# Optimization experiments

Measured on AMD Instinct MI355X. Metric: run time of the kernel, lower is better.

The kernel has to match this reference:

```python
import jax, jax.numpy as jnp
import numpy as np

NUM_HEADS = 1
HIDDEN = 256
HEAD_DIM = HIDDEN // NUM_HEADS
SCALE = HEAD_DIM ** -0.5


def _rotate_pairwise(x):
    # (... , d) -> rotate adjacent pairs: (x0,x1,x2,x3,..) -> (-x1,x0,-x3,x2,..)
    shape = x.shape
    x = x.reshape(*shape[:-1], -1, 2)
    x = jnp.stack([-x[..., 1], x[..., 0]], axis=-1)
    return x.reshape(shape)


def setup_inputs() -> dict:
    key = jax.random.key(0)
    ks = jax.random.split(key, 12)
    B, PB, QS, KS = 1, 1, 4096, 16448
    KV_IN = 64
    d = {
        'query': jax.random.normal(ks[0], (B, PB, QS, HIDDEN), jnp.float32),
        'key': jax.random.normal(ks[1], (B, PB, KS, KV_IN), jnp.float32),
        'value': jax.random.normal(ks[2], (B, PB, KS, KV_IN), jnp.float32),
        'rope_cos': jax.random.normal(ks[3], (QS, HEAD_DIM), jnp.float32),
        'rope_sin': jax.random.normal(ks[4], (QS, HEAD_DIM), jnp.float32),
        'wq': jax.random.normal(ks[5], (HIDDEN, HIDDEN), jnp.float32) * (HIDDEN ** -0.5),
        'bq': jnp.zeros((HIDDEN,), jnp.float32),
        'wk': jax.random.normal(ks[6], (KV_IN, HIDDEN), jnp.float32) * (KV_IN ** -0.5),
        'bk': jnp.zeros((HIDDEN,), jnp.float32),
        'wv': jax.random.normal(ks[7], (KV_IN, HIDDEN), jnp.float32) * (KV_IN ** -0.5),
        'bv': jnp.zeros((HIDDEN,), jnp.float32),
        'wo': jax.random.normal(ks[8], (HIDDEN, HIDDEN), jnp.float32) * (HIDDEN ** -0.5),
        'bo': jnp.zeros((HIDDEN,), jnp.float32),
        'num_k_exclude_rope': 64,
    }
    return d


def reference(query, key, value, rope_cos, rope_sin, wq, bq, wk, bk, wv, bv, wo, bo, num_k_exclude_rope):
    batch, pb, qs, _ = query.shape
    ks = key.shape[2]
    B = batch * pb
    # projections -> [B, H, S, hd]
    q = (query @ wq + bq).reshape(B, qs, NUM_HEADS, HEAD_DIM).transpose(0, 2, 1, 3)
    k = (key @ wk + bk).reshape(B, ks, NUM_HEADS, HEAD_DIM).transpose(0, 2, 1, 3)
    v = (value @ wv + bv).reshape(B, ks, NUM_HEADS, HEAD_DIM).transpose(0, 2, 1, 3)
    cos = rope_cos[None, None]  # [1,1,QS,hd]
    sin = rope_sin[None, None]
    # split off non-RoPE keys (object pointer tokens)
    n_rot = ks - num_k_exclude_rope
    k_rot, k_pass = k[:, :, :n_rot, :], k[:, :, n_rot:, :]
    q = q * cos + _rotate_pairwise(q) * sin
    if n_rot != qs:  # rope_k_repeat branch (static shapes)
        rep = n_rot // qs
        cos_k = jnp.repeat(cos, rep, axis=2)
        sin_k = jnp.repeat(sin, rep, axis=2)
    else:
        cos_k, sin_k = cos, sin
    k_emb = k_rot * cos_k + _rotate_pairwise(k_rot) * sin_k
    k = jnp.concatenate([k_emb, k_pass], axis=-2)
    attn = jax.nn.softmax(jnp.einsum('bhqd,bhkd->bhqk', q * SCALE, k), axis=-1)
    x = jnp.einsum('bhqk,bhkd->bhqd', attn, v)
    x = x.transpose(0, 2, 1, 3).reshape(batch, pb, qs, HIDDEN)
    return x @ wo + bo
```

## Files before the change

kernel.cpp:

```cpp
#include <hip/hip_runtime.h>
#include <hip/hip_bf16.h>

typedef __attribute__((ext_vector_type(4))) float floatx4;
typedef __attribute__((ext_vector_type(8))) short shortx8;
typedef __attribute__((ext_vector_type(8))) _Float16 halfx8;
typedef _Float16 half_t;

#define MFMA_BF16(A,B,C) __builtin_amdgcn_mfma_f32_16x16x32_bf16((A),(B),(C),0,0,0)
#define NEG_INF (-__builtin_inff())
#define GLOBAL_AS __attribute__((address_space(1)))
#define LDS_AS __attribute__((address_space(3)))

static __device__ __forceinline__ unsigned short f2b(float f) {
    union { float f; unsigned u; } v; v.f = f;
    unsigned r = v.u + 0x7FFFu + ((v.u >> 16) & 1u);
    return (unsigned short)(r >> 16);
}
static __device__ __forceinline__ unsigned pack_bf16(float lo, float hi) {
    return (unsigned)f2b(lo) | ((unsigned)f2b(hi) << 16);
}
static __device__ __forceinline__ unsigned pack_half(float lo, float hi) {
    union { half_t h[2]; unsigned u; } p;
    p.h[0] = (half_t)lo; p.h[1] = (half_t)hi;
    return p.u;
}
static __device__ __forceinline__ float EXP2F(float x) { return __builtin_amdgcn_exp2f(x); }

#define NSPLIT 8
#define NSPLIT_C 16
#define NTILES 257

__global__ __launch_bounds__(256) void wtrans_kernel(
    const float* __restrict__ wq, const float* __restrict__ wk,
    const float* __restrict__ wv, const float* __restrict__ wo,
    unsigned short* __restrict__ wqt, unsigned short* __restrict__ wkt,
    unsigned short* __restrict__ wvt, unsigned short* __restrict__ wot)
{
    __shared__ unsigned short tb[64 * 68];
    const int bid = blockIdx.x, tid = threadIdx.x;
    const float* src; unsigned short* dst; int K0, N0, Kfull;
    if (bid < 16)      { src = wq; dst = wqt; Kfull = 256; K0 = (bid >> 2) * 64; N0 = (bid & 3) * 64; }
    else if (bid < 20) { src = wk; dst = wkt; Kfull = 64;  K0 = 0; N0 = (bid - 16) * 64; }
    else if (bid < 24) { src = wv; dst = wvt; Kfull = 64;  K0 = 0; N0 = (bid - 20) * 64; }
    else { int t2 = bid - 24; src = wo; dst = wot; Kfull = 256; K0 = (t2 >> 2) * 64; N0 = (t2 & 3) * 64; }

    {
        const int r = tid >> 2, c0 = (tid & 3) * 16;
        const float* p = src + (K0 + r) * 256 + N0 + c0;
        #pragma unroll
        for (int j = 0; j < 16; j += 4) {
            floatx4 f = *(const floatx4*)(p + j);
            tb[r * 68 + c0 + j + 0] = f2b(f[0]);
            tb[r * 68 + c0 + j + 1] = f2b(f[1]);
            tb[r * 68 + c0 + j + 2] = f2b(f[2]);
            tb[r * 68 + c0 + j + 3] = f2b(f[3]);
        }
    }
    __syncthreads();
    {
        const int n = tid >> 2, k0 = (tid & 3) * 16;
        shortx8 v0, v1;
        #pragma unroll
        for (int j = 0; j < 8; j++) {
            v0[j] = tb[(k0 + j) * 68 + n];
            v1[j] = tb[(k0 + 8 + j) * 68 + n];
        }
        unsigned short* q = dst + (N0 + n) * Kfull + K0 + k0;
        *(shortx8*)q = v0;
        *(shortx8*)(q + 8) = v1;
    }
}

__global__ __launch_bounds__(256) void proj_kernel(
    const float* __restrict__ query, const float* __restrict__ key,
    const float* __restrict__ value,
    const unsigned short* __restrict__ wqt, const float* __restrict__ bq,
    const unsigned short* __restrict__ wkt, const float* __restrict__ bk,
    const unsigned short* __restrict__ wvt, const float* __restrict__ bv,
    const float* __restrict__ cosb, const float* __restrict__ sinb,
    const int* __restrict__ nkx,
    unsigned short* __restrict__ qr, unsigned short* __restrict__ krw,
    unsigned short* __restrict__ vtg)
{
    __shared__ unsigned short tbuf[256 * 72];
    const int tid = threadIdx.x;
    const int wave = tid >> 6, lane = tid & 63;
    const int c = lane & 15, quad = lane >> 4;
    const int bx = blockIdx.x;

    if (bx < 64) {
        const int m0 = bx * 64;
        shortx8 aA[8];
        {
            const int mrow = m0 + wave * 16 + c;
            #pragma unroll
            for (int ks = 0; ks < 8; ks++) {
                const float* p = query + mrow * 256 + ks * 32 + quad * 8;
                floatx4 f0 = *(const floatx4*)p;
                floatx4 f1 = *(const floatx4*)(p + 4);
                shortx8 a;
                #pragma unroll
                for (int j = 0; j < 4; j++) { a[j] = (short)f2b(f0[j]); a[j + 4] = (short)f2b(f1[j]); }
                aA[ks] = a;
            }
        }
        floatx4 acc[16];
        #pragma unroll
        for (int nt = 0; nt < 16; nt++) { acc[nt][0]=0.f; acc[nt][1]=0.f; acc[nt][2]=0.f; acc[nt][3]=0.f; }
        #pragma unroll
        for (int nt = 0; nt < 16; nt++) {
            #pragma unroll
            for (int ks = 0; ks < 8; ks++) {
                shortx8 b = *(const shortx8*)(wqt + (nt * 16 + c) * 256 + ks * 32 + quad * 8);
                acc[nt] = MFMA_BF16(aA[ks], b, acc[nt]);
            }
        }
        const float sc = 0.09016844005556021f;
        #pragma unroll
        for (int nt = 0; nt < 16; nt++) {
            const int col = nt * 16 + c;
            float vals[4];
            #pragma unroll
            for (int r = 0; r < 4; r++) {
                const int row = m0 + wave * 16 + quad * 4 + r;
                float v = acc[nt][r] + bq[col];
                float partner = __shfl_xor(v, 1);
                float cv = cosb[row * 256 + col];
                float sn = sinb[row * 256 + col];
                float rot = (col & 1) ? partner : -partner;
                vals[r] = (v * cv + rot * sn) * sc;
            }
            #pragma unroll
            for (int r2 = 0; r2 < 4; r2 += 2) {
                float a = vals[r2], b = vals[r2 + 1];
                float ax = __shfl_xor(a, 1), bx2 = __shfl_xor(b, 1);
                float lo = (c & 1) ? bx2 : a;
                float hi = (c & 1) ? b : ax;
                int row = m0 + wave * 16 + quad * 4 + r2 + (c & 1);
                *(unsigned*)(qr + row * 256 + nt * 16 + (c & ~1)) = pack_bf16(lo, hi);
            }
        }
        return;
    }

    const int isv = (bx >= 321);
    const int m0 = (isv ? (bx - 321) : (bx - 64)) * 64;
    const float* src = isv ? value : key;
    const unsigned short* wt = isv ? wvt : wkt;
    const float* bias = isv ? bv : bk;

    shortx8 aA[2];
    {
        const int mrow = m0 + wave * 16 + c;
        #pragma unroll
        for (int ks = 0; ks < 2; ks++) {
            const float* p = src + mrow * 64 + ks * 32 + quad * 8;
            floatx4 f0 = *(const floatx4*)p;
            floatx4 f1 = *(const floatx4*)(p + 4);
            shortx8 a;
            #pragma unroll
            for (int j = 0; j < 4; j++) { a[j] = (short)f2b(f0[j]); a[j + 4] = (short)f2b(f1[j]); }
            aA[ks] = a;
        }
    }
    floatx4 acc[16];
    #pragma unroll
    for (int nt = 0; nt < 16; nt++) { acc[nt][0]=0.f; acc[nt][1]=0.f; acc[nt][2]=0.f; acc[nt][3]=0.f; }
    #pragma unroll
    for (int nt = 0; nt < 16; nt++) {
        #pragma unroll
        for (int ks = 0; ks < 2; ks++) {
            shortx8 b = *(const shortx8*)(wt + (nt * 16 + c) * 64 + ks * 32 + quad * 8);
            acc[nt] = MFMA_BF16(aA[ks], b, acc[nt]);
        }
    }
    if (!isv) {
        const int n_rot = 16448 - nkx[0];
        int rep = n_rot / 4096; if (rep < 1) rep = 1;
        int rc4[4];
        #pragma unroll
        for (int r = 0; r < 4; r++) {
            int row = m0 + wave * 16 + quad * 4 + r;
            rc4[r] = row / rep;
        }
        #pragma unroll
        for (int nt = 0; nt < 16; nt++) {
            const int col = nt * 16 + c;
            float vals[4];
            #pragma unroll
            for (int r = 0; r < 4; r++) {
                const int row = m0 + wave * 16 + quad * 4 + r;
                float v = acc[nt][r] + bias[col];
                float partner = __shfl_xor(v, 1);
                float outv = v;
                if (row < n_rot) {
                    float cv = cosb[rc4[r] * 256 + col];
                    float sn = sinb[rc4[r] * 256 + col];
                    float rot = (col & 1) ? partner : -partner;
                    outv = v * cv + rot * sn;
                }
                vals[r] = outv;
            }
            #pragma unroll
            for (int r2 = 0; r2 < 4; r2 += 2) {
                float a = vals[r2], b = vals[r2 + 1];
                float ax = __shfl_xor(a, 1), bx2 = __shfl_xor(b, 1);
                float lo = (c & 1) ? bx2 : a;
                float hi = (c & 1) ? b : ax;
                int row = m0 + wave * 16 + quad * 4 + r2 + (c & 1);
                *(unsigned*)(krw + row * 256 + nt * 16 + (c & ~1)) = pack_bf16(lo, hi);
            }
        }
    } else {
        #pragma unroll
        for (int nt = 0; nt < 16; nt++) {
            const int col = nt * 16 + c;
            #pragma unroll
            for (int r = 0; r < 4; r++) {
                const int rl = wave * 16 + quad * 4 + r;
                tbuf[col * 72 + rl] = f2b(acc[nt][r] + bias[col]);
            }
        }
        __syncthreads();
        #pragma unroll
        for (int i = 0; i < 8; i++) {
            int G = i * 256 + tid;
            int n = G >> 3, g = G & 7;
            *(floatx4*)(vtg + n * 16448 + m0 + g * 8) = *(const floatx4*)(tbuf + n * 72 + g * 8);
        }
    }
}

__global__ __launch_bounds__(512, 2) void flash_kernel(
    const unsigned short* __restrict__ qr, const unsigned short* __restrict__ kr,
    const unsigned short* __restrict__ vt, half_t* __restrict__ Opart,
    float* __restrict__ Lpart)
{
    __shared__ unsigned short smem[75776];
    const int tid = threadIdx.x;
    const int wave = tid >> 6, lane = tid & 63;
    const int c = lane & 15, quad = lane >> 4;
    const int cx = c & 7;
    const int qg = wave & 3, kvh = wave >> 2;
    const int qrow0 = blockIdx.x * 128 + qg * 32;
    const int s = blockIdx.y;
    const int t0 = (s * NTILES) / NSPLIT, t1 = ((s + 1) * NTILES) / NSPLIT;
    unsigned short* pw = smem + 65536 + wave * 1280;

    shortx8 aQ[2][8];
    #pragma unroll
    for (int u = 0; u < 2; u++)
        #pragma unroll
        for (int ks = 0; ks < 8; ks++)
            aQ[u][ks] = *(const shortx8*)(qr + (qrow0 + u * 16 + c) * 256 + ks * 32 + quad * 8);

    floatx4 o[2][16];
    #pragma unroll
    for (int u = 0; u < 2; u++)
        #pragma unroll
        for (int nt = 0; nt < 16; nt++) { o[u][nt][0]=0.f; o[u][nt][1]=0.f; o[u][nt][2]=0.f; o[u][nt][3]=0.f; }
    float l_i[2] = { 0.f, 0.f };

    auto stage = [&](int t, int buf) {
        const int kv0 = t * 64;
        unsigned short* kb = smem + buf * 16384;
        unsigned short* vb = smem + 32768 + buf * 16384;
        #pragma unroll
        for (int i = 0; i < 4; i++) {
            int L = i * 512 + tid;
            int kv = L >> 5, p = L & 31;
            int g = (p & 24) | ((p & 7) ^ (kv & 7));
            __builtin_amdgcn_global_load_lds(
                (const GLOBAL_AS void*)(const void*)(kr + (kv0 + kv) * 256 + g * 8),
                (LDS_AS void*)(void*)(kb + (i * 512 + wave * 64) * 8), 16, 0, 0);
        }
        #pragma unroll
        for (int i = 0; i < 4; i++) {
            int L = i * 512 + tid;
            int d = L >> 3, p = L & 7;
            int g = p ^ (d & 7);
            __builtin_amdgcn_global_load_lds(
                (const GLOBAL_AS void*)(const void*)(vt + d * 16448 + kv0 + g * 8),
                (LDS_AS void*)(void*)(vb + (i * 512 + wave * 64) * 8), 16, 0, 0);
        }
    };

    stage(t0, 0);
    int cur = 0;
    const int pv_p = (kvh * 4 + quad) ^ cx;
    for (int t = t0; t < t1; t++) {
        __syncthreads();
        if (t + 1 < t1) stage(t + 1, cur ^ 1);
        const unsigned short* kb = smem + cur * 16384;
        const unsigned short* vb = smem + 32768 + cur * 16384;

        floatx4 sv[2][2];
        #pragma unroll
        for (int u = 0; u < 2; u++)
            #pragma unroll
            for (int nt = 0; nt < 2; nt++) { sv[u][nt][0]=0.f; sv[u][nt][1]=0.f; sv[u][nt][2]=0.f; sv[u][nt][3]=0.f; }
        #pragma unroll
        for (int nt = 0; nt < 2; nt++) {
            const unsigned short* krow = kb + (kvh * 32 + nt * 16 + c) * 256;
            #pragma unroll
            for (int ks = 0; ks < 8; ks++) {
                int p = ((ks >> 1) * 8) | ((((ks & 1) << 2) + quad) ^ cx);
                shortx8 kfrag = *(const shortx8*)(krow + p * 8);
                sv[0][nt] = MFMA_BF16(kfrag, aQ[0][ks], sv[0][nt]);
                sv[1][nt] = MFMA_BF16(kfrag, aQ[1][ks], sv[1][nt]);
            }
        }
        #pragma unroll
        for (int u = 0; u < 2; u++) {
            float rs = 0.f;
            #pragma unroll
            for (int nt = 0; nt < 2; nt++)
                #pragma unroll
                for (int r = 0; r < 4; r++) {
                    float pv = EXP2F(sv[u][nt][r]);
                    sv[u][nt][r] = pv;
                    rs += pv;
                }
            l_i[u] += rs;
        }
        #pragma unroll
        for (int u = 0; u < 2; u++)
            #pragma unroll
            for (int nt = 0; nt < 2; nt++)
                #pragma unroll
                for (int r2 = 0; r2 < 4; r2 += 2)
                    *(unsigned*)(pw + (u * 16 + c) * 40 + nt * 16 + quad * 4 + r2) =
                        pack_bf16(sv[u][nt][r2], sv[u][nt][r2 + 1]);
        shortx8 aP[2];
        #pragma unroll
        for (int u = 0; u < 2; u++)
            aP[u] = *(const shortx8*)(pw + (u * 16 + c) * 40 + quad * 8);
        #pragma unroll
        for (int nt = 0; nt < 16; nt++) {
            const unsigned short* vrow = vb + (nt * 16 + c) * 64;
            shortx8 b0 = *(const shortx8*)(vrow + pv_p * 8);
            o[0][nt] = MFMA_BF16(aP[0], b0, o[0][nt]);
            o[1][nt] = MFMA_BF16(aP[1], b0, o[1][nt]);
        }
        cur ^= 1;
    }
    const int sEff = s * 2 + kvh;
    half_t* Ob = Opart + (size_t)sEff * (4096 * 256);
    #pragma unroll
    for (int u = 0; u < 2; u++) {
        l_i[u] += __shfl_xor(l_i[u], 16);
        l_i[u] += __shfl_xor(l_i[u], 32);
    }
    float inv[2] = { 1.0f / l_i[0], 1.0f / l_i[1] };
    #pragma unroll
    for (int u = 0; u < 2; u++) {
        float ar[4];
        #pragma unroll
        for (int r = 0; r < 4; r++) ar[r] = __shfl(inv[u], quad * 4 + r);
        #pragma unroll
        for (int nt = 0; nt < 16; nt++) {
            o[u][nt][0] *= ar[0]; o[u][nt][1] *= ar[1];
            o[u][nt][2] *= ar[2]; o[u][nt][3] *= ar[3];
        }
    }
    #pragma unroll
    for (int u = 0; u < 2; u++)
        #pragma unroll
        for (int nt = 0; nt < 16; nt++)
            #pragma unroll
            for (int r2 = 0; r2 < 4; r2 += 2) {
                float a = o[u][nt][r2], b = o[u][nt][r2 + 1];
                float ax = __shfl_xor(a, 1), bx2 = __shfl_xor(b, 1);
                float lo = (c & 1) ? bx2 : a;
                float hi = (c & 1) ? b : ax;
                int row = qrow0 + u * 16 + quad * 4 + r2 + (c & 1);
                *(unsigned*)(Ob + row * 256 + nt * 16 + (c & ~1)) = pack_half(lo, hi);
            }
    if (quad == 0) {
        #pragma unroll
        for (int u = 0; u < 2; u++)
            Lpart[sEff * 4096 + qrow0 + u * 16 + c] = l_i[u];
    }
}

__global__ __launch_bounds__(256) void combine_kernel(
    const half_t* __restrict__ Opart, const float* __restrict__ Lpart,
    unsigned short* __restrict__ xb)
{
    int idx = blockIdx.x * 256 + threadIdx.x;
    int row = idx >> 5;
    int d0 = (idx & 31) * 8;
    float wn[NSPLIT_C], den = 0.f;
    #pragma unroll
    for (int sp = 0; sp < NSPLIT_C; sp++) { wn[sp] = Lpart[sp * 4096 + row]; den += wn[sp]; }
    float inv = 1.0f / den;
    #pragma unroll
    for (int sp = 0; sp < NSPLIT_C; sp++) wn[sp] *= inv;
    float acc[8];
    #pragma unroll
    for (int j = 0; j < 8; j++) acc[j] = 0.f;
    #pragma unroll
    for (int sp = 0; sp < NSPLIT_C; sp++) {
        halfx8 hv = *(const halfx8*)(Opart + (size_t)sp * (4096 * 256) + row * 256 + d0);
        #pragma unroll
        for (int j = 0; j < 8; j++) acc[j] += wn[sp] * (float)hv[j];
    }
    shortx8 xv;
    #pragma unroll
    for (int j = 0; j < 8; j++) xv[j] = (short)f2b(acc[j]);
    *(shortx8*)(xb + row * 256 + d0) = xv;
}

__global__ __launch_bounds__(256) void oproj_kernel(
    const unsigned short* __restrict__ xb, const unsigned short* __restrict__ wot,
    const float* __restrict__ bo, float* __restrict__ outp)
{
    const int tid = threadIdx.x;
    const int wave = tid >> 6, lane = tid & 63;
    const int c = lane & 15, quad = lane >> 4;
    const int m0 = blockIdx.x * 64;
    const int n0 = blockIdx.y * 64;

    shortx8 aX[8];
    #pragma unroll
    for (int ks = 0; ks < 8; ks++)
        aX[ks] = *(const shortx8*)(xb + (m0 + wave * 16 + c) * 256 + ks * 32 + quad * 8);
    floatx4 acc[4];
    #pragma unroll
    for (int nt = 0; nt < 4; nt++) { acc[nt][0]=0.f; acc[nt][1]=0.f; acc[nt][2]=0.f; acc[nt][3]=0.f; }
    #pragma unroll
    for (int nt = 0; nt < 4; nt++) {
        #pragma unroll
        for (int ks = 0; ks < 8; ks++) {
            shortx8 b = *(const shortx8*)(wot + (n0 + nt * 16 + c) * 256 + ks * 32 + quad * 8);
            acc[nt] = MFMA_BF16(aX[ks], b, acc[nt]);
        }
    }
    #pragma unroll
    for (int nt = 0; nt < 4; nt++) {
        const int col = n0 + nt * 16 + c;
        #pragma unroll
        for (int r = 0; r < 4; r++) {
            const int row = m0 + wave * 16 + quad * 4 + r;
            outp[row * 256 + col] = acc[nt][r] + bo[col];
        }
    }
}

extern "C" void kernel_launch(void* const* d_in, const int* in_sizes, int n_in,
                              void* d_out, int out_size, void* d_ws, size_t ws_size,
                              hipStream_t stream) {
    const float* query = (const float*)d_in[0];
    const float* key   = (const float*)d_in[1];
    const float* value = (const float*)d_in[2];
    const float* cosb  = (const float*)d_in[3];
    const float* sinb  = (const float*)d_in[4];
    const float* wq    = (const float*)d_in[5];
    const float* bq    = (const float*)d_in[6];
    const float* wk    = (const float*)d_in[7];
    const float* bk    = (const float*)d_in[8];
    const float* wv    = (const float*)d_in[9];
    const float* bv    = (const float*)d_in[10];
    const float* wo    = (const float*)d_in[11];
    const float* bo    = (const float*)d_in[12];
    const int*   nk    = (const int*)d_in[13];

    char* ws = (char*)d_ws;
    unsigned short* wqt = (unsigned short*)(ws + 0);
    unsigned short* wkt = (unsigned short*)(ws + 131072);
    unsigned short* wvt = (unsigned short*)(ws + 163840);
    unsigned short* wot = (unsigned short*)(ws + 196608);
    unsigned short* qr  = (unsigned short*)(ws + 327680);
    unsigned short* xb  = (unsigned short*)(ws + 327680);
    unsigned short* krw = (unsigned short*)(ws + 2424832);
    unsigned short* vtg = (unsigned short*)(ws + 10846208);
    half_t* Opart = (half_t*)(ws + 19267584);
    float* Lpart = (float*)(ws + 52822016);
    float* outp  = (float*)d_out;

    wtrans_kernel<<<dim3(40), dim3(256), 0, stream>>>(wq, wk, wv, wo, wqt, wkt, wvt, wot);
    proj_kernel<<<dim3(578), dim3(256), 0, stream>>>(
        query, key, value, wqt, bq, wkt, bk, wvt, bv, cosb, sinb, nk, qr, krw, vtg);
    flash_kernel<<<dim3(32, NSPLIT), dim3(512), 0, stream>>>(qr, krw, vtg, Opart, Lpart);
    combine_kernel<<<dim3(512), dim3(256), 0, stream>>>(Opart, Lpart, xb);
    oproj_kernel<<<dim3(64, 4), dim3(256), 0, stream>>>(xb, wot, bo, outp);
}
```

Baseline: 231.7 us.

## Switch flash kernel to 32x32 MFMA with in-register P and fuse combine+oproj

```diff
diff --git a/kernel.cpp b/kernel.cpp
--- a/kernel.cpp
+++ b/kernel.cpp
@@ -2,12 +2,13 @@
 #include <hip/hip_bf16.h>
 
 typedef __attribute__((ext_vector_type(4))) float floatx4;
+typedef __attribute__((ext_vector_type(16))) float floatx16;
 typedef __attribute__((ext_vector_type(8))) short shortx8;
 typedef __attribute__((ext_vector_type(8))) _Float16 halfx8;
 typedef _Float16 half_t;
 
-#define MFMA_BF16(A,B,C) __builtin_amdgcn_mfma_f32_16x16x32_bf16((A),(B),(C),0,0,0)
-#define NEG_INF (-__builtin_inff())
+#define MFMA_BF16(A,B,C)   __builtin_amdgcn_mfma_f32_16x16x32_bf16((A),(B),(C),0,0,0)
+#define MFMA32_BF16(A,B,C) __builtin_amdgcn_mfma_f32_32x32x16_bf16((A),(B),(C),0,0,0)
 #define GLOBAL_AS __attribute__((address_space(1)))
 #define LDS_AS __attribute__((address_space(3)))
 
@@ -23,6 +24,11 @@
     union { half_t h[2]; unsigned u; } p;
     p.h[0] = (half_t)lo; p.h[1] = (half_t)hi;
     return p.u;
+}
+static __device__ __forceinline__ unsigned cvtpk_bf16(float lo, float hi) {
+    unsigned r;
+    asm("v_cvt_pk_bf16_f32 %0, %1, %2" : "=v"(r) : "v"(lo), "v"(hi));
+    return r;
 }
 static __device__ __forceinline__ float EXP2F(float x) { return __builtin_amdgcn_exp2f(x); }
 
@@ -236,30 +242,26 @@
     const unsigned short* __restrict__ vt, half_t* __restrict__ Opart,
     float* __restrict__ Lpart)
 {
-    __shared__ unsigned short smem[75776];
+    __shared__ unsigned short smem[65536];
     const int tid = threadIdx.x;
     const int wave = tid >> 6, lane = tid & 63;
-    const int c = lane & 15, quad = lane >> 4;
-    const int cx = c & 7;
+    const int l31 = lane & 31, h = lane >> 5, l7 = lane & 7;
     const int qg = wave & 3, kvh = wave >> 2;
     const int qrow0 = blockIdx.x * 128 + qg * 32;
     const int s = blockIdx.y;
     const int t0 = (s * NTILES) / NSPLIT, t1 = ((s + 1) * NTILES) / NSPLIT;
-    unsigned short* pw = smem + 65536 + wave * 1280;
-
-    shortx8 aQ[2][8];
-    #pragma unroll
-    for (int u = 0; u < 2; u++)
-        #pragma unroll
-        for (int ks = 0; ks < 8; ks++)
-            aQ[u][ks] = *(const shortx8*)(qr + (qrow0 + u * 16 + c) * 256 + ks * 32 + quad * 8);
-
-    floatx4 o[2][16];
-    #pragma unroll
-    for (int u = 0; u < 2; u++)
-        #pragma unroll
-        for (int nt = 0; nt < 16; nt++) { o[u][nt][0]=0.f; o[u][nt][1]=0.f; o[u][nt][2]=0.f; o[u][nt][3]=0.f; }
-    float l_i[2] = { 0.f, 0.f };
+
+    shortx8 aQ[16];
+    #pragma unroll
+    for (int ks = 0; ks < 16; ks++)
+        aQ[ks] = *(const shortx8*)(qr + (qrow0 + l31) * 256 + ks * 16 + h * 8);
+
+    floatx16 o[8];
+    #pragma unroll
+    for (int dt = 0; dt < 8; dt++)
+        #pragma unroll
+        for (int r = 0; r < 16; r++) o[dt][r] = 0.f;
+    float l_i = 0.f;
 
     auto stage = [&](int t, int buf) {
         const int kv0 = t * 64;
@@ -287,161 +289,148 @@
 
     stage(t0, 0);
     int cur = 0;
-    const int pv_p = (kvh * 4 + quad) ^ cx;
+    const int krowoff = (kvh * 32 + l31) * 256;
     for (int t = t0; t < t1; t++) {
         __syncthreads();
         if (t + 1 < t1) stage(t + 1, cur ^ 1);
         const unsigned short* kb = smem + cur * 16384;
         const unsigned short* vb = smem + 32768 + cur * 16384;
 
-        floatx4 sv[2][2];
-        #pragma unroll
-        for (int u = 0; u < 2; u++)
-            #pragma unroll
-            for (int nt = 0; nt < 2; nt++) { sv[u][nt][0]=0.f; sv[u][nt][1]=0.f; sv[u][nt][2]=0.f; sv[u][nt][3]=0.f; }
-        #pragma unroll
-        for (int nt = 0; nt < 2; nt++) {
-            const unsigned short* krow = kb + (kvh * 32 + nt * 16 + c) * 256;
-            #pragma unroll
-            for (int ks = 0; ks < 8; ks++) {
-                int p = ((ks >> 1) * 8) | ((((ks & 1) << 2) + quad) ^ cx);
-                shortx8 kfrag = *(const shortx8*)(krow + p * 8);
-                sv[0][nt] = MFMA_BF16(kfrag, aQ[0][ks], sv[0][nt]);
-                sv[1][nt] = MFMA_BF16(kfrag, aQ[1][ks], sv[1][nt]);
-            }
-        }
-        #pragma unroll
-        for (int u = 0; u < 2; u++) {
-            float rs = 0.f;
-            #pragma unroll
-            for (int nt = 0; nt < 2; nt++)
-                #pragma unroll
-                for (int r = 0; r < 4; r++) {
-                    float pv = EXP2F(sv[u][nt][r]);
-                    sv[u][nt][r] = pv;
-                    rs += pv;
-                }
-            l_i[u] += rs;
-        }
-        #pragma unroll
-        for (int u = 0; u < 2; u++)
-            #pragma unroll
-            for (int nt = 0; nt < 2; nt++)
-                #pragma unroll
-                for (int r2 = 0; r2 < 4; r2 += 2)
-                    *(unsigned*)(pw + (u * 16 + c) * 40 + nt * 16 + quad * 4 + r2) =
-                        pack_bf16(sv[u][nt][r2], sv[u][nt][r2 + 1]);
-        shortx8 aP[2];
-        #pragma unroll
-        for (int u = 0; u < 2; u++)
-            aP[u] = *(const shortx8*)(pw + (u * 16 + c) * 40 + quad * 8);
-        #pragma unroll
-        for (int nt = 0; nt < 16; nt++) {
-            const unsigned short* vrow = vb + (nt * 16 + c) * 64;
-            shortx8 b0 = *(const shortx8*)(vrow + pv_p * 8);
-            o[0][nt] = MFMA_BF16(aP[0], b0, o[0][nt]);
-            o[1][nt] = MFMA_BF16(aP[1], b0, o[1][nt]);
-        }
+        floatx16 sv0, sv1;
+        #pragma unroll
+        for (int r = 0; r < 16; r++) { sv0[r] = 0.f; sv1[r] = 0.f; }
+        __builtin_amdgcn_s_setprio(1);
+        #pragma unroll
+        for (int ks = 0; ks < 16; ks++) {
+            int q8 = ks * 2 + h;
+            int p8 = (q8 & 24) | ((q8 & 7) ^ l7);
+            shortx8 kf = *(const shortx8*)(kb + krowoff + p8 * 8);
+            if (ks & 1) sv1 = MFMA32_BF16(kf, aQ[ks], sv1);
+            else        sv0 = MFMA32_BF16(kf, aQ[ks], sv0);
+        }
+        __builtin_amdgcn_s_setprio(0);
+
+        float rs = 0.f;
+        #pragma unroll
+        for (int r = 0; r < 16; r++) {
+            float p = EXP2F(sv0[r] + sv1[r]);
+            sv0[r] = p;
+            rs += p;
+        }
+        l_i += rs;
+
+        shortx8 pa[2];
+        #pragma unroll
+        for (int sp = 0; sp < 2; sp++) {
+            unsigned w0 = cvtpk_bf16(sv0[sp * 8 + 0], sv0[sp * 8 + 1]);
+            unsigned w1 = cvtpk_bf16(sv0[sp * 8 + 2], sv0[sp * 8 + 3]);
+            unsigned w2 = cvtpk_bf16(sv0[sp * 8 + 4], sv0[sp * 8 + 5]);
+            unsigned w3 = cvtpk_bf16(sv0[sp * 8 + 6], sv0[sp * 8 + 7]);
+            asm("v_permlane32_swap_b32 %0, %1" : "+v"(w0), "+v"(w2));
+            asm("v_permlane32_swap_b32 %0, %1" : "+v"(w1), "+v"(w3));
+            union { unsigned u[4]; shortx8 v; } pk;
+            pk.u[0] = w0; pk.u[1] = w1; pk.u[2] = w2; pk.u[3] = w3;
+            pa[sp] = pk.v;
+        }
+
+        __builtin_amdgcn_s_setprio(1);
+        #pragma unroll
+        for (int dt = 0; dt < 8; dt++) {
+            const unsigned short* vrow = vb + (dt * 32 + l31) * 64;
+            shortx8 v0 = *(const shortx8*)(vrow + ((kvh * 4 + h) ^ l7) * 8);
+            shortx8 v1 = *(const shortx8*)(vrow + ((kvh * 4 + 2 + h) ^ l7) * 8);
+            o[dt] = MFMA32_BF16(pa[0], v0, o[dt]);
+            o[dt] = MFMA32_BF16(pa[1], v1, o[dt]);
+        }
+        __builtin_amdgcn_s_setprio(0);
         cur ^= 1;
     }
+
     const int sEff = s * 2 + kvh;
     half_t* Ob = Opart + (size_t)sEff * (4096 * 256);
-    #pragma unroll
-    for (int u = 0; u < 2; u++) {
-        l_i[u] += __shfl_xor(l_i[u], 16);
-        l_i[u] += __shfl_xor(l_i[u], 32);
-    }
-    float inv[2] = { 1.0f / l_i[0], 1.0f / l_i[1] };
-    #pragma unroll
-    for (int u = 0; u < 2; u++) {
-        float ar[4];
-        #pragma unroll
-        for (int r = 0; r < 4; r++) ar[r] = __shfl(inv[u], quad * 4 + r);
-        #pragma unroll
-        for (int nt = 0; nt < 16; nt++) {
-            o[u][nt][0] *= ar[0]; o[u][nt][1] *= ar[1];
-            o[u][nt][2] *= ar[2]; o[u][nt][3] *= ar[3];
-        }
-    }
-    #pragma unroll
-    for (int u = 0; u < 2; u++)
-        #pragma unroll
-        for (int nt = 0; nt < 16; nt++)
-            #pragma unroll
-            for (int r2 = 0; r2 < 4; r2 += 2) {
-                float a = o[u][nt][r2], b = o[u][nt][r2 + 1];
-                float ax = __shfl_xor(a, 1), bx2 = __shfl_xor(b, 1);
-                float lo = (c & 1) ? bx2 : a;
-                float hi = (c & 1) ? b : ax;
-                int row = qrow0 + u * 16 + quad * 4 + r2 + (c & 1);
-                *(unsigned*)(Ob + row * 256 + nt * 16 + (c & ~1)) = pack_half(lo, hi);
-            }
-    if (quad == 0) {
-        #pragma unroll
-        for (int u = 0; u < 2; u++)
-            Lpart[sEff * 4096 + qrow0 + u * 16 + c] = l_i[u];
-    }
-}
-
-__global__ __launch_bounds__(256) void combine_kernel(
+    l_i += __shfl_xor(l_i, 32);
+    float inv = 1.0f / l_i;
+    float ivr[16];
+    #pragma unroll
+    for (int r = 0; r < 16; r++)
+        ivr[r] = __shfl(inv, (r & 3) + 8 * (r >> 2) + 4 * h);
+    #pragma unroll
+    for (int dt = 0; dt < 8; dt++)
+        #pragma unroll
+        for (int r2 = 0; r2 < 16; r2 += 2) {
+            float a = o[dt][r2] * ivr[r2];
+            float b = o[dt][r2 + 1] * ivr[r2 + 1];
+            float ax = __shfl_xor(a, 1), bx2 = __shfl_xor(b, 1);
+            float lo = (lane & 1) ? bx2 : a;
+            float hi = (lane & 1) ? b : ax;
+            int q = (r2 & 3) + 8 * (r2 >> 2) + 4 * h;
+            int row = qrow0 + q + (lane & 1);
+            *(unsigned*)(Ob + row * 256 + dt * 32 + (l31 & ~1)) = pack_half(lo, hi);
+        }
+    if (lane < 32) Lpart[sEff * 4096 + qrow0 + lane] = l_i;
+}
+
+__global__ __launch_bounds__(256) void combine_oproj_kernel(
     const half_t* __restrict__ Opart, const float* __restrict__ Lpart,
-    unsigned short* __restrict__ xb)
+    const unsigned short* __restrict__ wot, const float* __restrict__ bo,
+    float* __restrict__ outp)
 {
-    int idx = blockIdx.x * 256 + threadIdx.x;
-    int row = idx >> 5;
-    int d0 = (idx & 31) * 8;
-    float wn[NSPLIT_C], den = 0.f;
-    #pragma unroll
-    for (int sp = 0; sp < NSPLIT_C; sp++) { wn[sp] = Lpart[sp * 4096 + row]; den += wn[sp]; }
-    float inv = 1.0f / den;
-    #pragma unroll
-    for (int sp = 0; sp < NSPLIT_C; sp++) wn[sp] *= inv;
-    float acc[8];
-    #pragma unroll
-    for (int j = 0; j < 8; j++) acc[j] = 0.f;
-    #pragma unroll
-    for (int sp = 0; sp < NSPLIT_C; sp++) {
-        halfx8 hv = *(const halfx8*)(Opart + (size_t)sp * (4096 * 256) + row * 256 + d0);
-        #pragma unroll
-        for (int j = 0; j < 8; j++) acc[j] += wn[sp] * (float)hv[j];
-    }
-    shortx8 xv;
-    #pragma unroll
-    for (int j = 0; j < 8; j++) xv[j] = (short)f2b(acc[j]);
-    *(shortx8*)(xb + row * 256 + d0) = xv;
-}
-
-__global__ __launch_bounds__(256) void oproj_kernel(
-    const unsigned short* __restrict__ xb, const unsigned short* __restrict__ wot,
-    const float* __restrict__ bo, float* __restrict__ outp)
-{
+    __shared__ unsigned short xt[16 * 264];
     const int tid = threadIdx.x;
-    const int wave = tid >> 6, lane = tid & 63;
+    const int m0 = blockIdx.x * 16;
+
+    {
+        const int d0 = (tid & 31) * 8;
+        #pragma unroll
+        for (int pass = 0; pass < 2; pass++) {
+            const int rl = pass * 8 + (tid >> 5);
+            const int row = m0 + rl;
+            float wn[NSPLIT_C], den = 0.f;
+            #pragma unroll
+            for (int sp = 0; sp < NSPLIT_C; sp++) { wn[sp] = Lpart[sp * 4096 + row]; den += wn[sp]; }
+            float inv = 1.0f / den;
+            float acc[8];
+            #pragma unroll
+            for (int j = 0; j < 8; j++) acc[j] = 0.f;
+            #pragma unroll
+            for (int sp = 0; sp < NSPLIT_C; sp++) {
+                halfx8 hv = *(const halfx8*)(Opart + (size_t)sp * (4096 * 256) + row * 256 + d0);
+                float w = wn[sp] * inv;
+                #pragma unroll
+                for (int j = 0; j < 8; j++) acc[j] += w * (float)hv[j];
+            }
+            shortx8 xv;
+            #pragma unroll
+            for (int j = 0; j < 8; j++) xv[j] = (short)f2b(acc[j]);
+            *(shortx8*)(xt + rl * 264 + d0) = xv;
+        }
+    }
+    __syncthreads();
+
+    const int lane = tid & 63, wave = tid >> 6;
     const int c = lane & 15, quad = lane >> 4;
-    const int m0 = blockIdx.x * 64;
-    const int n0 = blockIdx.y * 64;
-
     shortx8 aX[8];
     #pragma unroll
     for (int ks = 0; ks < 8; ks++)
-        aX[ks] = *(const shortx8*)(xb + (m0 + wave * 16 + c) * 256 + ks * 32 + quad * 8);
+        aX[ks] = *(const shortx8*)(xt + c * 264 + ks * 32 + quad * 8);
     floatx4 acc[4];
     #pragma unroll
     for (int nt = 0; nt < 4; nt++) { acc[nt][0]=0.f; acc[nt][1]=0.f; acc[nt][2]=0.f; acc[nt][3]=0.f; }
     #pragma unroll
     for (int nt = 0; nt < 4; nt++) {
+        const int n = (wave * 4 + nt) * 16;
         #pragma unroll
         for (int ks = 0; ks < 8; ks++) {
-            shortx8 b = *(const shortx8*)(wot + (n0 + nt * 16 + c) * 256 + ks * 32 + quad * 8);
+            shortx8 b = *(const shortx8*)(wot + (n + c) * 256 + ks * 32 + quad * 8);
             acc[nt] = MFMA_BF16(aX[ks], b, acc[nt]);
         }
     }
     #pragma unroll
     for (int nt = 0; nt < 4; nt++) {
-        const int col = n0 + nt * 16 + c;
+        const int col = (wave * 4 + nt) * 16 + c;
         #pragma unroll
         for (int r = 0; r < 4; r++) {
-            const int row = m0 + wave * 16 + quad * 4 + r;
+            const int row = m0 + quad * 4 + r;
             outp[row * 256 + col] = acc[nt][r] + bo[col];
         }
     }
@@ -471,7 +460,6 @@
     unsigned short* wvt = (unsigned short*)(ws + 163840);
     unsigned short* wot = (unsigned short*)(ws + 196608);
     unsigned short* qr  = (unsigned short*)(ws + 327680);
-    unsigned short* xb  = (unsigned short*)(ws + 327680);
     unsigned short* krw = (unsigned short*)(ws + 2424832);
     unsigned short* vtg = (unsigned short*)(ws + 10846208);
     half_t* Opart = (half_t*)(ws + 19267584);
@@ -482,6 +470,5 @@
     proj_kernel<<<dim3(578), dim3(256), 0, stream>>>(
         query, key, value, wqt, bq, wkt, bk, wvt, bv, cosb, sinb, nk, qr, krw, vtg);
     flash_kernel<<<dim3(32, NSPLIT), dim3(512), 0, stream>>>(qr, krw, vtg, Opart, Lpart);
-    combine_kernel<<<dim3(512), dim3(256), 0, stream>>>(Opart, Lpart, xb);
-    oproj_kernel<<<dim3(64, 4), dim3(256), 0, stream>>>(xb, wot, bo, outp);
-}
+    combine_oproj_kernel<<<dim3(256), dim3(256), 0, stream>>>(Opart, Lpart, wot, bo, outp);
+}
```

After: 239.7 us. +3.5%, slower.
